# Kernel tuning notes

Hardware: AMD Instinct MI355X
Metric: run time of the kernel (lower is better)

Reference implementation:

```python
import jax, jax.numpy as jnp
import numpy as np

ALPHA, GAMMA = 0.25, 2.0
COST_CLASS, COST_BBOX, COST_GIOU = 2.0, 5.0, 2.0
EPS = 1e-8


def box_cxcywh_to_xyxy(b):
    cx, cy, w, h = b[..., 0], b[..., 1], b[..., 2], b[..., 3]
    return jnp.stack([cx - 0.5 * w, cy - 0.5 * h, cx + 0.5 * w, cy + 0.5 * h], axis=-1)


def generalized_box_iou(boxes1, boxes2):
    # boxes1: [N,4] xyxy, boxes2: [M,4] xyxy -> [N,M] GIoU
    area1 = (boxes1[:, 2] - boxes1[:, 0]) * (boxes1[:, 3] - boxes1[:, 1])
    area2 = (boxes2[:, 2] - boxes2[:, 0]) * (boxes2[:, 3] - boxes2[:, 1])
    lt = jnp.maximum(boxes1[:, None, :2], boxes2[None, :, :2])   # [N,M,2]
    rb = jnp.minimum(boxes1[:, None, 2:], boxes2[None, :, 2:])   # [N,M,2]
    wh = jnp.clip(rb - lt, 0.0)
    inter = wh[..., 0] * wh[..., 1]
    union = area1[:, None] + area2[None, :] - inter
    iou = inter / union
    # smallest enclosing box
    lt_c = jnp.minimum(boxes1[:, None, :2], boxes2[None, :, :2])
    rb_c = jnp.maximum(boxes1[:, None, 2:], boxes2[None, :, 2:])
    wh_c = jnp.clip(rb_c - lt_c, 0.0)
    area_c = wh_c[..., 0] * wh_c[..., 1]
    return iou - (area_c - union) / area_c


def setup_inputs() -> dict:
    key = jax.random.key(0)
    k1, k2, k3, k4 = jax.random.split(key, 4)
    BS, NQ, NC, NT = 16, 900, 91, 960
    pred_logits = jax.random.normal(k1, (BS, NQ, NC), dtype=jnp.float32)
    pred_boxes = jax.random.uniform(k2, (BS, NQ, 4), dtype=jnp.float32)
    tgt_ids = jax.random.randint(k3, (NT,), 0, NC, dtype=jnp.int64)
    tgt_bbox = jax.random.uniform(k4, (NT, 4), dtype=jnp.float32)
    return {"pred_logits": pred_logits, "pred_boxes": pred_boxes,
            "tgt_ids": tgt_ids, "tgt_bbox": tgt_bbox}


def reference(pred_logits, pred_boxes, tgt_ids, tgt_bbox):
    bs, nq, _ = pred_logits.shape
    out_prob = jax.nn.sigmoid(pred_logits.reshape(bs * nq, -1))      # [BN, C]
    out_bbox = pred_boxes.reshape(bs * nq, 4)                         # [BN, 4]
    # focal-style classification cost, gathered at target class ids
    neg_cost = (1.0 - ALPHA) * out_prob ** GAMMA * (-jnp.log(1.0 - out_prob + EPS))
    pos_cost = ALPHA * (1.0 - out_prob) ** GAMMA * (-jnp.log(out_prob + EPS))
    cost_class = pos_cost[:, tgt_ids] - neg_cost[:, tgt_ids]          # [BN, NT]
    # pairwise L1 distance between boxes (cxcywh space), like torch.cdist(p=1)
    cost_bbox = jnp.sum(jnp.abs(out_bbox[:, None, :] - tgt_bbox[None, :, :]), axis=-1)
    cost_giou = -generalized_box_iou(box_cxcywh_to_xyxy(out_bbox),
                                     box_cxcywh_to_xyxy(tgt_bbox))    # [BN, NT]
    C = COST_BBOX * cost_bbox + COST_CLASS * cost_class + COST_GIOU * cost_giou
    return C.reshape(bs, nq, -1)
```

## Files before the change

### kernel.cpp

```cpp
#include <hip/hip_runtime.h>
#include <math.h>


#define ALPHA_F   0.25f
#define COST_CLS  2.0f
#define COST_BBOX 5.0f
#define COST_GIOU 2.0f
#define EPS_F     1e-8f

constexpr int THREADS = 256;

template<int NC, int NT, int ROWS>
__global__ __launch_bounds__(THREADS, 6) void matcher_kernel_s(
    const float* __restrict__ logits,
    const float* __restrict__ boxes,
    const int*   __restrict__ tids,
    const float* __restrict__ tboxes,
    float*       __restrict__ out)
{
    constexpr int CLS_STRIDE = 96;
    constexpr int JPT = 4;
    constexpr int NJT = NT / JPT;
    constexpr int NTAB = ROWS * NC;
    constexpr int LPT  = (NTAB + THREADS - 1) / THREADS;
    __shared__ float s_cls[ROWS * CLS_STRIDE];

    const int tid  = threadIdx.x;
    const int row0 = blockIdx.x * ROWS;
    const bool active = tid < NJT;

    float tcx[JPT], tcy[JPT], tw[JPT], th[JPT];
    float tx0[JPT], tx1[JPT], ty0[JPT], ty1[JPT], tarea[JPT];
    const float* cp[JPT];
    if (active) {
        const int4 tv = reinterpret_cast<const int4*>(tids)[tid];
        const int ic[JPT] = {tv.x, tv.y, tv.z, tv.w};
        #pragma unroll
        for (int k = 0; k < JPT; ++k) {
            const float4 b = reinterpret_cast<const float4*>(tboxes)[tid * JPT + k];
            tcx[k] = b.x; tcy[k] = b.y; tw[k] = b.z; th[k] = b.w;
            const float hw = 0.5f * b.z, hh = 0.5f * b.w;
            tx0[k] = b.x - hw;  tx1[k] = b.x + hw;
            ty0[k] = b.y - hh;  ty1[k] = b.y + hh;
            tarea[k] = b.z * b.w;
            cp[k] = s_cls + ic[k];
        }
    } else {
        #pragma unroll
        for (int k = 0; k < JPT; ++k) {
            tcx[k]=tcy[k]=tw[k]=th[k]=tx0[k]=tx1[k]=ty0[k]=ty1[k]=tarea[k]=0.f;
            cp[k] = s_cls;
        }
    }

    const float* __restrict__ lg = logits + (size_t)row0 * NC;
    #pragma unroll
    for (int i = 0; i < LPT; ++i) {
        const int t = tid + i * THREADS;
        if (t < NTAB) {
            const float x  = lg[t];
            const float p  = 1.0f / (1.0f + __expf(-x));
            const float om = 1.0f - p;
            const float neg = (1.0f - ALPHA_F) * p * p * (-__logf(om + EPS_F));
            const float pos = ALPHA_F * om * om        * (-__logf(p  + EPS_F));
            const int r = t / NC, c = t - r * NC;
            s_cls[r * CLS_STRIDE + c] = pos - neg;
        }
    }
    __syncthreads();

    if (!active) return;

    float* __restrict__ optr = out + (size_t)row0 * NT + tid * JPT;
    #pragma unroll
    for (int r = 0; r < ROWS; ++r) {
        const float4 pb = reinterpret_cast<const float4*>(boxes)[row0 + r];
        const float px0 = pb.x - 0.5f * pb.z, py0 = pb.y - 0.5f * pb.w;
        const float px1 = pb.x + 0.5f * pb.z, py1 = pb.y + 0.5f * pb.w;
        const float parea = pb.z * pb.w;

        float rv[JPT];
        #pragma unroll
        for (int k = 0; k < JPT; ++k) {
            const float l1 = (fabsf(pb.x - tcx[k]) + fabsf(pb.y - tcy[k]))
                           + (fabsf(pb.z - tw[k])  + fabsf(pb.w - th[k]));
            const float iwr = fminf(px1, tx1[k]) - fmaxf(px0, tx0[k]);
            const float ihr = fminf(py1, ty1[k]) - fmaxf(py0, ty0[k]);
            const float inter = fmaxf(iwr, 0.0f) * fmaxf(ihr, 0.0f);
            const float uni = (parea + tarea[k]) - inter;
            const float cw = (pb.z + tw[k]) - iwr;
            const float ch = (pb.w + th[k]) - ihr;
            const float carea = cw * ch;
            const float num  = carea * (inter - uni) + uni * uni;
            const float giou = num * __builtin_amdgcn_rcpf(uni * carea);
            const float ccls = cp[k][r * CLS_STRIDE];
            rv[k] = (COST_BBOX * l1 + COST_CLS * ccls) - COST_GIOU * giou;
        }
        *reinterpret_cast<float4*>(optr) = make_float4(rv[0], rv[1], rv[2], rv[3]);
        optr += NT;
    }
}

constexpr int GROWS = 8;
__global__ __launch_bounds__(THREADS) void matcher_kernel_g(
    const float* __restrict__ logits, const float* __restrict__ boxes,
    const int* __restrict__ tids, const float* __restrict__ tboxes,
    float* __restrict__ out, int BN, int NC, int NT)
{
    extern __shared__ float s_cls_g[];
    const int tid  = threadIdx.x;
    const int row0 = blockIdx.x * GROWS;
    const int nrows = (BN - row0 < GROWS) ? (BN - row0) : GROWS;

    for (int t = tid; t < nrows * NC; t += THREADS) {
        const int r = t / NC, c = t - r * NC;
        const float x  = logits[(size_t)(row0 + r) * NC + c];
        const float p  = 1.0f / (1.0f + expf(-x));
        const float om = 1.0f - p;
        const float neg = (1.0f - ALPHA_F) * p * p * (-logf(om + EPS_F));
        const float pos = ALPHA_F * om * om        * (-logf(p + EPS_F));
        s_cls_g[r * NC + c] = pos - neg;
    }
    __syncthreads();

    for (int r = 0; r < nrows; ++r) {
        const int row = row0 + r;
        const float4 pb = reinterpret_cast<const float4*>(boxes)[row];
        const float px0 = pb.x - 0.5f * pb.z, py0 = pb.y - 0.5f * pb.w;
        const float px1 = pb.x + 0.5f * pb.z, py1 = pb.y + 0.5f * pb.w;
        const float parea = pb.z * pb.w;
        for (int j = tid; j < NT; j += THREADS) {
            const float4 b = reinterpret_cast<const float4*>(tboxes)[j];
            const float bx0 = b.x - 0.5f * b.z, by0 = b.y - 0.5f * b.w;
            const float bx1 = b.x + 0.5f * b.z, by1 = b.y + 0.5f * b.w;
            const float l1 = fabsf(pb.x - b.x) + fabsf(pb.y - b.y)
                           + fabsf(pb.z - b.z) + fabsf(pb.w - b.w);
            const float iw = fmaxf(fminf(px1, bx1) - fmaxf(px0, bx0), 0.0f);
            const float ih = fmaxf(fminf(py1, by1) - fmaxf(py0, by0), 0.0f);
            const float inter = iw * ih;
            const float uni = parea + b.z * b.w - inter;
            const float iou = inter / uni;
            const float cw = fmaxf(px1, bx1) - fminf(px0, bx0);
            const float ch = fmaxf(py1, by1) - fminf(py0, by0);
            const float carea = cw * ch;
            const float giou = iou - (carea - uni) / carea;
            const float ccls = s_cls_g[r * NC + tids[j]];
            out[(size_t)row * NT + j] = COST_BBOX * l1 + COST_CLS * ccls - COST_GIOU * giou;
        }
        __syncthreads();
    }
}

extern "C" void kernel_launch(void* const* d_in, const int* in_sizes, int n_in,
                              void* d_out, int out_size, void* d_ws, size_t ws_size,
                              hipStream_t stream) {
    const float* logits = (const float*)d_in[0];
    const float* boxes  = (const float*)d_in[1];
    const int*   tids   = (const int*)d_in[2];
    const float* tboxes = (const float*)d_in[3];
    float* out = (float*)d_out;

    const int BN = in_sizes[1] / 4;
    const int NC = in_sizes[0] / BN;
    const int NT = in_sizes[2];

    constexpr int ROWS = 4;
    if (NC == 91 && NT == 960 && BN % ROWS == 0) {
        const int grid = BN / ROWS;
        matcher_kernel_s<91, 960, ROWS><<<grid, THREADS, 0, stream>>>(
            logits, boxes, tids, tboxes, out);
    } else {
        const int grid = (BN + GROWS - 1) / GROWS;
        const size_t shmem = (size_t)GROWS * NC * sizeof(float);
        matcher_kernel_g<<<grid, THREADS, shmem, stream>>>(
            logits, boxes, tids, tboxes, out, BN, NC, NT);
    }
}
```

Measured before the change: 23.82 us.

## Transpose class-cost table to class-major float4 and prefetch logits early

The shared class-cost table is stored class-major as float4, so each thread fetches all four rows' costs for a target with one 16-byte LDS read instead of four scalar reads. Logit loads are issued at kernel start, before the target-box setup, so global latency overlaps that work. Prediction boxes for all rows are also loaded before the row loop. In exchange the kernel holds more registers, and the class-major layout may cause LDS bank conflicts on the writes.

```diff
diff --git a/kernel.cpp b/kernel.cpp
--- a/kernel.cpp
+++ b/kernel.cpp
@@ -10,7 +10,7 @@
 
 constexpr int THREADS = 256;
 
-template<int NC, int NT, int ROWS>
+template<int NC, int NT>
 __global__ __launch_bounds__(THREADS, 6) void matcher_kernel_s(
     const float* __restrict__ logits,
     const float* __restrict__ boxes,
@@ -18,23 +18,34 @@
     const float* __restrict__ tboxes,
     float*       __restrict__ out)
 {
-    constexpr int CLS_STRIDE = 96;
-    constexpr int JPT = 4;
-    constexpr int NJT = NT / JPT;
+    constexpr int ROWS = 4;
+    constexpr int JPT  = 4;
+    constexpr int NJT  = NT / JPT;
     constexpr int NTAB = ROWS * NC;
     constexpr int LPT  = (NTAB + THREADS - 1) / THREADS;
-    __shared__ float s_cls[ROWS * CLS_STRIDE];
+    constexpr int NCP  = 96;
+
+    __shared__ float4 s_cls4[NCP];
+    float* const s_clsf = reinterpret_cast<float*>(s_cls4);
 
     const int tid  = threadIdx.x;
     const int row0 = blockIdx.x * ROWS;
     const bool active = tid < NJT;
 
+    const float* __restrict__ lg = logits + (size_t)row0 * NC;
+    float lv[LPT];
+    #pragma unroll
+    for (int i = 0; i < LPT; ++i) {
+        const int t = tid + i * THREADS;
+        lv[i] = (t < NTAB) ? lg[t] : 0.0f;
+    }
+
     float tcx[JPT], tcy[JPT], tw[JPT], th[JPT];
     float tx0[JPT], tx1[JPT], ty0[JPT], ty1[JPT], tarea[JPT];
-    const float* cp[JPT];
+    int   ic[JPT];
     if (active) {
         const int4 tv = reinterpret_cast<const int4*>(tids)[tid];
-        const int ic[JPT] = {tv.x, tv.y, tv.z, tv.w};
+        ic[0] = tv.x; ic[1] = tv.y; ic[2] = tv.z; ic[3] = tv.w;
         #pragma unroll
         for (int k = 0; k < JPT; ++k) {
             const float4 b = reinterpret_cast<const float4*>(tboxes)[tid * JPT + k];
@@ -43,38 +54,46 @@
             tx0[k] = b.x - hw;  tx1[k] = b.x + hw;
             ty0[k] = b.y - hh;  ty1[k] = b.y + hh;
             tarea[k] = b.z * b.w;
-            cp[k] = s_cls + ic[k];
         }
     } else {
         #pragma unroll
         for (int k = 0; k < JPT; ++k) {
             tcx[k]=tcy[k]=tw[k]=th[k]=tx0[k]=tx1[k]=ty0[k]=ty1[k]=tarea[k]=0.f;
-            cp[k] = s_cls;
+            ic[k] = 0;
         }
     }
 
-    const float* __restrict__ lg = logits + (size_t)row0 * NC;
     #pragma unroll
     for (int i = 0; i < LPT; ++i) {
         const int t = tid + i * THREADS;
         if (t < NTAB) {
-            const float x  = lg[t];
+            const float x  = lv[i];
             const float p  = 1.0f / (1.0f + __expf(-x));
             const float om = 1.0f - p;
             const float neg = (1.0f - ALPHA_F) * p * p * (-__logf(om + EPS_F));
             const float pos = ALPHA_F * om * om        * (-__logf(p  + EPS_F));
             const int r = t / NC, c = t - r * NC;
-            s_cls[r * CLS_STRIDE + c] = pos - neg;
+            s_clsf[c * ROWS + r] = pos - neg;
         }
     }
     __syncthreads();
 
     if (!active) return;
 
+    float4 cc[JPT];
+    #pragma unroll
+    for (int k = 0; k < JPT; ++k)
+        cc[k] = s_cls4[ic[k]];
+
+    float4 pbv[ROWS];
+    #pragma unroll
+    for (int r = 0; r < ROWS; ++r)
+        pbv[r] = reinterpret_cast<const float4*>(boxes)[row0 + r];
+
     float* __restrict__ optr = out + (size_t)row0 * NT + tid * JPT;
     #pragma unroll
     for (int r = 0; r < ROWS; ++r) {
-        const float4 pb = reinterpret_cast<const float4*>(boxes)[row0 + r];
+        const float4 pb = pbv[r];
         const float px0 = pb.x - 0.5f * pb.z, py0 = pb.y - 0.5f * pb.w;
         const float px1 = pb.x + 0.5f * pb.z, py1 = pb.y + 0.5f * pb.w;
         const float parea = pb.z * pb.w;
@@ -93,7 +112,8 @@
             const float carea = cw * ch;
             const float num  = carea * (inter - uni) + uni * uni;
             const float giou = num * __builtin_amdgcn_rcpf(uni * carea);
-            const float ccls = cp[k][r * CLS_STRIDE];
+            const float ccls = (r == 0) ? cc[k].x : (r == 1) ? cc[k].y
+                             : (r == 2) ? cc[k].z : cc[k].w;
             rv[k] = (COST_BBOX * l1 + COST_CLS * ccls) - COST_GIOU * giou;
         }
         *reinterpret_cast<float4*>(optr) = make_float4(rv[0], rv[1], rv[2], rv[3]);
@@ -164,10 +184,9 @@
     const int NC = in_sizes[0] / BN;
     const int NT = in_sizes[2];
 
-    constexpr int ROWS = 4;
-    if (NC == 91 && NT == 960 && BN % ROWS == 0) {
-        const int grid = BN / ROWS;
-        matcher_kernel_s<91, 960, ROWS><<<grid, THREADS, 0, stream>>>(
+    if (NC == 91 && NT == 960 && BN % 4 == 0) {
+        const int grid = BN / 4;
+        matcher_kernel_s<91, 960><<<grid, THREADS, 0, stream>>>(
             logits, boxes, tids, tboxes, out);
     } else {
         const int grid = (BN + GROWS - 1) / GROWS;
```

After: 23.89 us. About the same (+0.3%).

## Process eight rows per block, transpose class table, fold cost constants

Applied to the files above, without the earlier changes.

Each block now handles eight query rows instead of four, so the per-thread target-box setup is spread over twice as many output rows. The class-cost table in shared memory is transposed to class-major with a stride of 9, so each thread reads the eight rows of one class contiguously. Logits are loaded into registers before the target setup so the global loads overlap with that work. The class weight and the constant GIoU term are folded into the table, which removes a few FMAs per output element. The trade-off is half as many blocks and a launch-bounds occupancy hint that no longer asks for six blocks per CU, which could lower occupancy on a write-bound kernel.

```diff
diff --git a/kernel.cpp b/kernel.cpp
--- a/kernel.cpp
+++ b/kernel.cpp
@@ -10,24 +10,34 @@
 
 constexpr int THREADS = 256;
 
-template<int NC, int NT, int ROWS>
-__global__ __launch_bounds__(THREADS, 6) void matcher_kernel_s(
+template<int NC, int NT>
+__global__ __launch_bounds__(THREADS) void matcher_kernel_s(
     const float* __restrict__ logits,
     const float* __restrict__ boxes,
     const int*   __restrict__ tids,
     const float* __restrict__ tboxes,
     float*       __restrict__ out)
 {
-    constexpr int CLS_STRIDE = 96;
-    constexpr int JPT = 4;
-    constexpr int NJT = NT / JPT;
+    constexpr int ROWS = 8;
+    constexpr int JPT  = 4;
+    constexpr int NJT  = NT / JPT;
     constexpr int NTAB = ROWS * NC;
     constexpr int LPT  = (NTAB + THREADS - 1) / THREADS;
-    __shared__ float s_cls[ROWS * CLS_STRIDE];
+    constexpr int CSTR = 9;
+
+    __shared__ float s_cls[NC * CSTR];
 
     const int tid  = threadIdx.x;
     const int row0 = blockIdx.x * ROWS;
     const bool active = tid < NJT;
+
+    const float* __restrict__ lg = logits + (size_t)row0 * NC;
+    float lv[LPT];
+    #pragma unroll
+    for (int i = 0; i < LPT; ++i) {
+        const int t = tid + i * THREADS;
+        lv[i] = (t < NTAB) ? lg[t] : 0.0f;
+    }
 
     float tcx[JPT], tcy[JPT], tw[JPT], th[JPT];
     float tx0[JPT], tx1[JPT], ty0[JPT], ty1[JPT], tarea[JPT];
@@ -43,7 +53,7 @@
             tx0[k] = b.x - hw;  tx1[k] = b.x + hw;
             ty0[k] = b.y - hh;  ty1[k] = b.y + hh;
             tarea[k] = b.z * b.w;
-            cp[k] = s_cls + ic[k];
+            cp[k] = s_cls + ic[k] * CSTR;
         }
     } else {
         #pragma unroll
@@ -53,18 +63,17 @@
         }
     }
 
-    const float* __restrict__ lg = logits + (size_t)row0 * NC;
     #pragma unroll
     for (int i = 0; i < LPT; ++i) {
         const int t = tid + i * THREADS;
         if (t < NTAB) {
-            const float x  = lg[t];
+            const float x  = lv[i];
             const float p  = 1.0f / (1.0f + __expf(-x));
             const float om = 1.0f - p;
             const float neg = (1.0f - ALPHA_F) * p * p * (-__logf(om + EPS_F));
             const float pos = ALPHA_F * om * om        * (-__logf(p  + EPS_F));
             const int r = t / NC, c = t - r * NC;
-            s_cls[r * CLS_STRIDE + c] = pos - neg;
+            s_cls[c * CSTR + r] = COST_CLS * (pos - neg) + COST_GIOU;
         }
     }
     __syncthreads();
@@ -82,6 +91,7 @@
         float rv[JPT];
         #pragma unroll
         for (int k = 0; k < JPT; ++k) {
+            const float ctab = cp[k][r];
             const float l1 = (fabsf(pb.x - tcx[k]) + fabsf(pb.y - tcy[k]))
                            + (fabsf(pb.z - tw[k])  + fabsf(pb.w - th[k]));
             const float iwr = fminf(px1, tx1[k]) - fmaxf(px0, tx0[k]);
@@ -91,10 +101,10 @@
             const float cw = (pb.z + tw[k]) - iwr;
             const float ch = (pb.w + th[k]) - ihr;
             const float carea = cw * ch;
-            const float num  = carea * (inter - uni) + uni * uni;
-            const float giou = num * __builtin_amdgcn_rcpf(uni * carea);
-            const float ccls = cp[k][r * CLS_STRIDE];
-            rv[k] = (COST_BBOX * l1 + COST_CLS * ccls) - COST_GIOU * giou;
+            const float num  = fmaf(inter, carea, uni * uni);
+            const float rcpd = __builtin_amdgcn_rcpf(uni * carea);
+            const float base = fmaf(COST_BBOX, l1, ctab);
+            rv[k] = fmaf(-2.0f * num, rcpd, base);
         }
         *reinterpret_cast<float4*>(optr) = make_float4(rv[0], rv[1], rv[2], rv[3]);
         optr += NT;
@@ -164,10 +174,9 @@
     const int NC = in_sizes[0] / BN;
     const int NT = in_sizes[2];
 
-    constexpr int ROWS = 4;
-    if (NC == 91 && NT == 960 && BN % ROWS == 0) {
-        const int grid = BN / ROWS;
-        matcher_kernel_s<91, 960, ROWS><<<grid, THREADS, 0, stream>>>(
+    if (NC == 91 && NT == 960 && BN % 8 == 0) {
+        const int grid = BN / 8;
+        matcher_kernel_s<91, 960><<<grid, THREADS, 0, stream>>>(
             logits, boxes, tids, tboxes, out);
     } else {
         const int grid = (BN + GROWS - 1) / GROWS;
```

Result: slower. 24.83 us (+4.3%).
